# Optimization experiments

Measured on AMD Instinct MI355X. Metric: run time of the kernel, lower is better.

The kernel has to match this reference:

```python
import jax, jax.numpy as jnp
import numpy as np
from math import sqrt

B, L, S, H, E, D = 2, 2048, 2048, 16, 64, 64

def setup_inputs() -> dict:
    key = jax.random.key(0)
    kq, kk, kv = jax.random.split(key, 3)
    queries = jax.random.normal(kq, (B, L, H, E), dtype=jnp.float32)
    keys = jax.random.normal(kk, (B, S, H, E), dtype=jnp.float32)
    values = jax.random.normal(kv, (B, S, H, D), dtype=jnp.float32)
    # causal mask: True where attention is NOT allowed (j > i), matching masked_fill_ semantics
    causal = jnp.triu(jnp.ones((L, S), dtype=jnp.bool_), k=1)
    attn_mask = jnp.broadcast_to(causal[None, None, :, :], (B, 1, L, S))
    return {"queries": queries, "keys": keys, "values": values, "attn_mask": attn_mask}

def reference(queries, keys, values, attn_mask):
    # scores: [B,H,L,S]
    scale = 1.0 / sqrt(queries.shape[-1])
    scores = jnp.einsum('blhe,bshe->bhls', queries, keys)
    scores = jnp.where(attn_mask, -jnp.inf, scores)
    A = jax.nn.softmax(scale * scores, axis=-1)
    V = jnp.einsum('bhls,bshd->blhd', A, values)
    return V
```

## Files before the change

### kernel.cpp

```cpp
#include <hip/hip_runtime.h>

typedef unsigned short ushort_t;
typedef __attribute__((ext_vector_type(8))) short s8v;
typedef __attribute__((ext_vector_type(2))) unsigned u2v;
typedef __attribute__((ext_vector_type(4))) float f4;

__device__ __forceinline__ ushort_t f2bf(float x) {
    unsigned u = __builtin_bit_cast(unsigned, x);
    return (ushort_t)((u + 0x7FFFu + ((u >> 16) & 1u)) >> 16);
}
__device__ __forceinline__ unsigned pack_hi16(float lo, float hi) {
    unsigned a = __builtin_bit_cast(unsigned, lo);
    unsigned b = __builtin_bit_cast(unsigned, hi);
    return (a >> 16) | (b & 0xFFFF0000u);
}

__global__ __launch_bounds__(256) void prep_kv(const float* __restrict__ K,
                                               const float* __restrict__ V,
                                               ushort_t* __restrict__ Kb,
                                               ushort_t* __restrict__ VT) {
    __shared__ ushort_t T[64 * 72];
    if (blockIdx.x < 2048) {
        const int gid = blockIdx.x * 256 + threadIdx.x;
        const int e = (gid & 7) * 8;
        const int h = (gid >> 3) & 15;
        const int s = (gid >> 7) & 2047;
        const int b = gid >> 18;
        const float* src = K + (((b * 2048 + s) * 16 + h) * 64 + e);
        f4 a = *(const f4*)src;
        f4 c = *(const f4*)(src + 4);
        s8v o;
        #pragma unroll
        for (int j = 0; j < 4; ++j) { o[j] = (short)f2bf(a[j]); o[j + 4] = (short)f2bf(c[j]); }
        *(s8v*)(Kb + (((b * 16 + h) * 2048 + s) * 64 + e)) = o;
    } else {
        const int v = blockIdx.x - 2048;
        const int s0 = (v & 31) * 64;
        const int h  = (v >> 5) & 15;
        const int b  = v >> 9;
        const int t  = threadIdx.x;
        {
            const int srow = t >> 2, dc = (t & 3) * 16;
            const float* src = V + (((b * 2048 + s0 + srow) * 16 + h) * 64 + dc);
            #pragma unroll
            for (int c = 0; c < 4; ++c) {
                f4 vv = *(const f4*)(src + c * 4);
                #pragma unroll
                for (int j = 0; j < 4; ++j) T[(dc + c * 4 + j) * 72 + srow] = f2bf(vv[j]);
            }
        }
        __syncthreads();
        {
            const int d = t >> 2, sq = (t & 3) * 16;
            ushort_t* dst = VT + (((b * 16 + h) * 64 + d) * 2048 + s0 + sq);
            *(s8v*)(dst)     = *(const s8v*)(&T[d * 72 + sq]);
            *(s8v*)(dst + 8) = *(const s8v*)(&T[d * 72 + sq + 8]);
        }
    }
}

__global__ __launch_bounds__(256, 4) void fattn_main(
    const float* __restrict__ Q,
    const ushort_t* __restrict__ Kb,
    const ushort_t* __restrict__ VTb,
    float* __restrict__ O)
{
    constexpr float K1 = 0.18033688011112042f;
    constexpr float SHIFT = 12.0f;
    __shared__ ushort_t P[8][16 * 72];
    __shared__ float Obuf[32 * 64];
    __shared__ float Lbuf[32];

    const int bx = blockIdx.x;
    const int bh = bx & 31;
    const int pr = bx >> 5;
    const int b = bh >> 4, h = bh & 15;

    const int wave = threadIdx.x >> 6;
    const int lane = threadIdx.x & 63;
    const int l15  = lane & 15;
    const int quad = lane >> 4;

    const ushort_t* kb  = Kb  + bh * (2048 * 64);
    const ushort_t* vtb = VTb + bh * (64 * 2048);
    const float*    qb  = Q + b * (2048 * 1024) + h * 64;
    float*          ob  = O + b * (2048 * 1024) + h * 64;

    const s8v ones = {0x3F80, 0x3F80, 0x3F80, 0x3F80, 0x3F80, 0x3F80, 0x3F80, 0x3F80};
    const f4 zero4 = {0.f, 0.f, 0.f, 0.f};

    for (int half = 0; half < 2; ++half) {
        const int i   = half ? (63 - pr) : pr;
        const int qr0 = i * 32;
        const int il  = i >> 1;

        s8v aq[2][2];
        #pragma unroll
        for (int m = 0; m < 2; ++m) {
            const float* qrow = qb + (qr0 + m * 16 + l15) * 1024;
            #pragma unroll
            for (int ks = 0; ks < 2; ++ks) {
                f4 x = *(const f4*)(qrow + ks * 32 + quad * 8);
                f4 y = *(const f4*)(qrow + ks * 32 + quad * 8 + 4);
                #pragma unroll
                for (int j = 0; j < 4; ++j) {
                    aq[m][ks][j]     = (short)f2bf(x[j]);
                    aq[m][ks][j + 4] = (short)f2bf(y[j]);
                }
            }
        }

        f4 oacc[2][4];
        f4 lsum[2] = {zero4, zero4};
        #pragma unroll
        for (int m = 0; m < 2; ++m)
            #pragma unroll
            for (int d = 0; d < 4; ++d) oacc[m][d] = zero4;

        for (int it = wave; it <= il; it += 4) {
            const int n0 = it * 64;
            const ushort_t* kp = kb + n0 * 64;
            const ushort_t* vp = vtb + n0;

            s8v bk[4][2];
            #pragma unroll
            for (int t = 0; t < 4; ++t)
                #pragma unroll
                for (int ks = 0; ks < 2; ++ks)
                    bk[t][ks] = *(const s8v*)(kp + (t * 16 + l15) * 64 + ks * 32 + quad * 8);
            s8v bv[4][2];
            #pragma unroll
            for (int dd = 0; dd < 4; ++dd)
                #pragma unroll
                for (int ks = 0; ks < 2; ++ks)
                    bv[dd][ks] = *(const s8v*)(vp + (dd * 16 + l15) * 2048 + ks * 32 + quad * 8);

            const bool diag = (it == il);

            #pragma unroll
            for (int m = 0; m < 2; ++m) {
                ushort_t* Pm = P[wave * 2 + m];
                #pragma unroll
                for (int t = 0; t < 4; ++t) {
                    f4 a  = __builtin_amdgcn_mfma_f32_16x16x32_bf16(bk[t][0], aq[m][0], zero4, 0, 0, 0);
                    f4 st = __builtin_amdgcn_mfma_f32_16x16x32_bf16(bk[t][1], aq[m][1], a, 0, 0, 0);
                    float p[4];
                    #pragma unroll
                    for (int r = 0; r < 4; ++r) {
                        float x = __builtin_fmaf(st[r], K1, -SHIFT);
                        if (diag) {
                            const int gj = n0 + t * 16 + quad * 4 + r;
                            const int gi = qr0 + m * 16 + l15;
                            if (gj > gi) x = -INFINITY;
                        }
                        p[r] = __builtin_exp2f(x);
                    }
                    u2v pk;
                    pk[0] = pack_hi16(p[0], p[1]);
                    pk[1] = pack_hi16(p[2], p[3]);
                    *(u2v*)&Pm[l15 * 72 + t * 16 + quad * 4] = pk;
                }
            }

            #pragma unroll
            for (int m = 0; m < 2; ++m) {
                const ushort_t* Pm = P[wave * 2 + m];
                #pragma unroll
                for (int ks = 0; ks < 2; ++ks) {
                    const s8v ap = *(const s8v*)&Pm[l15 * 72 + ks * 32 + quad * 8];
                    lsum[m] = __builtin_amdgcn_mfma_f32_16x16x32_bf16(ap, ones, lsum[m], 0, 0, 0);
                    #pragma unroll
                    for (int dd = 0; dd < 4; ++dd)
                        oacc[m][dd] = __builtin_amdgcn_mfma_f32_16x16x32_bf16(ap, bv[dd][ks], oacc[m][dd], 0, 0, 0);
                }
            }
        }

        __syncthreads();
        #pragma unroll
        for (int w = 0; w < 4; ++w) {
            if (wave == w) {
                #pragma unroll
                for (int m = 0; m < 2; ++m) {
                    #pragma unroll
                    for (int dd = 0; dd < 4; ++dd)
                        #pragma unroll
                        for (int r = 0; r < 4; ++r) {
                            const int idx = (m * 16 + quad * 4 + r) * 64 + dd * 16 + l15;
                            if (w == 0) Obuf[idx] = oacc[m][dd][r];
                            else        Obuf[idx] += oacc[m][dd][r];
                        }
                    if (l15 == 0)
                        #pragma unroll
                        for (int r = 0; r < 4; ++r) {
                            const int row = m * 16 + quad * 4 + r;
                            if (w == 0) Lbuf[row] = lsum[m][r];
                            else        Lbuf[row] += lsum[m][r];
                        }
                }
            }
            __syncthreads();
        }
        {
            const int row = wave * 8 + (lane >> 3);
            const int c0  = (lane & 7) * 8;
            const float inv = 1.0f / Lbuf[row];
            f4 o0 = *(const f4*)&Obuf[row * 64 + c0];
            f4 o1 = *(const f4*)&Obuf[row * 64 + c0 + 4];
            #pragma unroll
            for (int j = 0; j < 4; ++j) { o0[j] *= inv; o1[j] *= inv; }
            float* dst = ob + (qr0 + row) * 1024 + c0;
            *(f4*)dst       = o0;
            *(f4*)(dst + 4) = o1;
        }
    }
}

#define PSTR 72
__global__ __launch_bounds__(256) void fattn_fallback(
    const float* __restrict__ Q, const float* __restrict__ K,
    const float* __restrict__ V, float* __restrict__ O)
{
    constexpr int strL = 1024, strB = 2048 * strL;
    const float scale = 0.125f;
    __shared__ ushort_t KT[64 * PSTR];
    __shared__ ushort_t VT[64 * PSTR];
    __shared__ ushort_t P[4][16 * PSTR];
    const int bh = blockIdx.x & 31;
    const int b = bh >> 4, h = bh & 15;
    const int im = 31 - (blockIdx.x >> 5);
    const int q0 = im * 64;
    const int tid = threadIdx.x, wave = tid >> 6, lane = tid & 63;
    const int l15 = lane & 15, quad = lane >> 4;
    const float* qbase = Q + b*strB + (q0 + wave*16 + l15)*strL + h*64;
    s8v aq0, aq1;
    {
        f4 q0v = *(const f4*)(qbase + quad*8);
        f4 q1v = *(const f4*)(qbase + quad*8 + 4);
        f4 q2v = *(const f4*)(qbase + 32 + quad*8);
        f4 q3v = *(const f4*)(qbase + 32 + quad*8 + 4);
        #pragma unroll
        for (int j = 0; j < 4; ++j) {
            aq0[j] = (short)f2bf(q0v[j]); aq0[j+4] = (short)f2bf(q1v[j]);
            aq1[j] = (short)f2bf(q2v[j]); aq1[j+4] = (short)f2bf(q3v[j]);
        }
    }
    const f4 zero4 = {0.f,0.f,0.f,0.f};
    f4 oacc[4]; float m_prev[4], lsum[4];
    #pragma unroll
    for (int d = 0; d < 4; ++d) oacc[d] = zero4;
    #pragma unroll
    for (int r = 0; r < 4; ++r) { m_prev[r] = -INFINITY; lsum[r] = 0.0f; }
    const float* kh = K + b*strB + h*64;
    const float* vh = V + b*strB + h*64;
    for (int it = 0; it <= im; ++it) {
        const int n0 = it * 64;
        __syncthreads();
        {
            const float* krow = kh + (n0 + lane)*strL + wave*16;
            f4 k0 = *(const f4*)(krow); f4 k1 = *(const f4*)(krow+4);
            f4 k2 = *(const f4*)(krow+8); f4 k3 = *(const f4*)(krow+12);
            s8v kb0, kb1;
            #pragma unroll
            for (int j = 0; j < 4; ++j) {
                kb0[j] = (short)f2bf(k0[j]); kb0[j+4] = (short)f2bf(k1[j]);
                kb1[j] = (short)f2bf(k2[j]); kb1[j+4] = (short)f2bf(k3[j]);
            }
            *(s8v*)&KT[lane*PSTR + wave*16] = kb0;
            *(s8v*)&KT[lane*PSTR + wave*16 + 8] = kb1;
            const float* vrow = vh + (n0 + lane)*strL + wave*16;
            f4 v0 = *(const f4*)(vrow); f4 v1 = *(const f4*)(vrow+4);
            f4 v2 = *(const f4*)(vrow+8); f4 v3 = *(const f4*)(vrow+12);
            #pragma unroll
            for (int j = 0; j < 4; ++j) {
                VT[(wave*16 + j)*PSTR + lane] = f2bf(v0[j]);
                VT[(wave*16 + 4 + j)*PSTR + lane] = f2bf(v1[j]);
                VT[(wave*16 + 8 + j)*PSTR + lane] = f2bf(v2[j]);
                VT[(wave*16 + 12 + j)*PSTR + lane] = f2bf(v3[j]);
            }
        }
        __syncthreads();
        f4 sacc[4];
        #pragma unroll
        for (int t = 0; t < 4; ++t) {
            sacc[t] = zero4;
            const s8v bk0 = *(const s8v*)&KT[(t*16 + l15)*PSTR + quad*8];
            const s8v bk1 = *(const s8v*)&KT[(t*16 + l15)*PSTR + 32 + quad*8];
            sacc[t] = __builtin_amdgcn_mfma_f32_16x16x32_bf16(aq0, bk0, sacc[t], 0, 0, 0);
            sacc[t] = __builtin_amdgcn_mfma_f32_16x16x32_bf16(aq1, bk1, sacc[t], 0, 0, 0);
        }
        const bool diag = (it == im);
        float sv[4][4], rmax[4];
        #pragma unroll
        for (int r = 0; r < 4; ++r) rmax[r] = -INFINITY;
        #pragma unroll
        for (int t = 0; t < 4; ++t)
            #pragma unroll
            for (int r = 0; r < 4; ++r) {
                float x = sacc[t][r] * scale;
                if (diag) {
                    const int gi = wave*16 + quad*4 + r;
                    const int gj = t*16 + l15;
                    if (gj > gi) x = -INFINITY;
                }
                sv[t][r] = x; rmax[r] = fmaxf(rmax[r], x);
            }
        #pragma unroll
        for (int off = 8; off >= 1; off >>= 1)
            #pragma unroll
            for (int r = 0; r < 4; ++r)
                rmax[r] = fmaxf(rmax[r], __shfl_xor(rmax[r], off, 64));
        float mnew[4], alpha[4], rsum[4];
        #pragma unroll
        for (int r = 0; r < 4; ++r) {
            mnew[r] = fmaxf(m_prev[r], rmax[r]);
            alpha[r] = __expf(m_prev[r] - mnew[r]);
            m_prev[r] = mnew[r]; rsum[r] = 0.f;
        }
        #pragma unroll
        for (int t = 0; t < 4; ++t)
            #pragma unroll
            for (int r = 0; r < 4; ++r) {
                const float p = __expf(sv[t][r] - mnew[r]);
                rsum[r] += p;
                P[wave][(quad*4 + r)*PSTR + t*16 + l15] = f2bf(p);
            }
        #pragma unroll
        for (int off = 8; off >= 1; off >>= 1)
            #pragma unroll
            for (int r = 0; r < 4; ++r)
                rsum[r] += __shfl_xor(rsum[r], off, 64);
        #pragma unroll
        for (int r = 0; r < 4; ++r) lsum[r] = alpha[r]*lsum[r] + rsum[r];
        #pragma unroll
        for (int d = 0; d < 4; ++d)
            #pragma unroll
            for (int r = 0; r < 4; ++r) oacc[d][r] *= alpha[r];
        #pragma unroll
        for (int ks = 0; ks < 2; ++ks) {
            const s8v ap = *(const s8v*)&P[wave][l15*PSTR + ks*32 + quad*8];
            #pragma unroll
            for (int d = 0; d < 4; ++d) {
                const s8v bvv = *(const s8v*)&VT[(d*16 + l15)*PSTR + ks*32 + quad*8];
                oacc[d] = __builtin_amdgcn_mfma_f32_16x16x32_bf16(ap, bvv, oacc[d], 0, 0, 0);
            }
        }
    }
    float* obase = O + b*strB + h*64;
    #pragma unroll
    for (int r = 0; r < 4; ++r) {
        const float inv = 1.0f / lsum[r];
        const int gi = q0 + wave*16 + quad*4 + r;
        #pragma unroll
        for (int d = 0; d < 4; ++d)
            obase[gi*strL + d*16 + l15] = oacc[d][r] * inv;
    }
}

extern "C" void kernel_launch(void* const* d_in, const int* in_sizes, int n_in,
                              void* d_out, int out_size, void* d_ws, size_t ws_size,
                              hipStream_t stream) {
    const float* Q = (const float*)d_in[0];
    const float* K = (const float*)d_in[1];
    const float* V = (const float*)d_in[2];
    float* O = (float*)d_out;
    const size_t NEED = 2ull * 4194304ull * 2ull;
    if (ws_size >= NEED) {
        ushort_t* Kb = (ushort_t*)d_ws;
        ushort_t* VT = Kb + 4194304;
        prep_kv<<<3072, 256, 0, stream>>>(K, V, Kb, VT);
        fattn_main<<<1024, 256, 0, stream>>>(Q, Kb, VT, O);
    } else {
        fattn_fallback<<<1024, 256, 0, stream>>>(Q, K, V, O);
    }
}
```

Before: 183.7 us.

## Share double-buffered K/V tiles in LDS across waves instead of splitting KV

The attention kernel changes from four waves each taking a strided subset of KV blocks (with a cross-wave reduction through shared memory) to two waves each owning 32 query rows of a 64-row tile. All waves now stream every KV block through double-buffered LDS tiles loaded cooperatively, with the next block prefetched while the current one is computed. The goal is to remove the Obuf/Lbuf reduction and its barriers, and to reuse each K/V load across more query rows. In exchange the grid has half as many blocks with 128 threads each, which lowers parallelism and occupancy. A barrier is also added on every KV iteration.

```diff
diff --git a/kernel.cpp b/kernel.cpp
--- a/kernel.cpp
+++ b/kernel.cpp
@@ -59,7 +59,7 @@
     }
 }
 
-__global__ __launch_bounds__(256, 4) void fattn_main(
+__global__ __launch_bounds__(128, 2) void fattn_main(
     const float* __restrict__ Q,
     const ushort_t* __restrict__ Kb,
     const ushort_t* __restrict__ VTb,
@@ -67,9 +67,9 @@
 {
     constexpr float K1 = 0.18033688011112042f;
     constexpr float SHIFT = 12.0f;
-    __shared__ ushort_t P[8][16 * 72];
-    __shared__ float Obuf[32 * 64];
-    __shared__ float Lbuf[32];
+    __shared__ ushort_t KT [2][64 * 72];
+    __shared__ ushort_t VTl[2][64 * 72];
+    __shared__ ushort_t P  [4][16 * 72];
 
     const int bx = blockIdx.x;
     const int bh = bx & 31;
@@ -89,15 +89,18 @@
     const s8v ones = {0x3F80, 0x3F80, 0x3F80, 0x3F80, 0x3F80, 0x3F80, 0x3F80, 0x3F80};
     const f4 zero4 = {0.f, 0.f, 0.f, 0.f};
 
+    const int sr = (wave << 5) + (lane >> 1);
+    const int sc = (lane & 1) << 5;
+
     for (int half = 0; half < 2; ++half) {
-        const int i   = half ? (63 - pr) : pr;
-        const int qr0 = i * 32;
-        const int il  = i >> 1;
+        const int i   = half ? (31 - pr) : pr;
+        const int qr0 = i * 64;
+        const int il  = i;
 
         s8v aq[2][2];
         #pragma unroll
         for (int m = 0; m < 2; ++m) {
-            const float* qrow = qb + (qr0 + m * 16 + l15) * 1024;
+            const float* qrow = qb + (qr0 + wave * 32 + m * 16 + l15) * 1024;
             #pragma unroll
             for (int ks = 0; ks < 2; ++ks) {
                 f4 x = *(const f4*)(qrow + ks * 32 + quad * 8);
@@ -117,40 +120,61 @@
             #pragma unroll
             for (int d = 0; d < 4; ++d) oacc[m][d] = zero4;
 
-        for (int it = wave; it <= il; it += 4) {
-            const int n0 = it * 64;
-            const ushort_t* kp = kb + n0 * 64;
-            const ushort_t* vp = vtb + n0;
-
-            s8v bk[4][2];
-            #pragma unroll
-            for (int t = 0; t < 4; ++t)
-                #pragma unroll
-                for (int ks = 0; ks < 2; ++ks)
-                    bk[t][ks] = *(const s8v*)(kp + (t * 16 + l15) * 64 + ks * 32 + quad * 8);
-            s8v bv[4][2];
-            #pragma unroll
-            for (int dd = 0; dd < 4; ++dd)
-                #pragma unroll
-                for (int ks = 0; ks < 2; ++ks)
-                    bv[dd][ks] = *(const s8v*)(vp + (dd * 16 + l15) * 2048 + ks * 32 + quad * 8);
-
+        {
+            const ushort_t* ksrc = kb + sr * 64 + sc;
+            ushort_t* kdst = &KT[0][sr * 72 + sc];
+            const ushort_t* vsrc = vtb + sr * 2048 + sc;
+            ushort_t* vdst = &VTl[0][sr * 72 + sc];
+            #pragma unroll
+            for (int c = 0; c < 4; ++c) {
+                *(s8v*)(kdst + c * 8) = *(const s8v*)(ksrc + c * 8);
+                *(s8v*)(vdst + c * 8) = *(const s8v*)(vsrc + c * 8);
+            }
+        }
+        __syncthreads();
+
+        for (int it = 0; it <= il; ++it) {
+            const int cur = it & 1;
+            const int n0  = it * 64;
             const bool diag = (it == il);
+
+            if (it < il) {
+                const int nn = (it + 1) * 64;
+                const ushort_t* ksrc = kb + (nn + sr) * 64 + sc;
+                ushort_t* kdst = &KT[cur ^ 1][sr * 72 + sc];
+                const ushort_t* vsrc = vtb + sr * 2048 + nn + sc;
+                ushort_t* vdst = &VTl[cur ^ 1][sr * 72 + sc];
+                #pragma unroll
+                for (int c = 0; c < 4; ++c) {
+                    *(s8v*)(kdst + c * 8) = *(const s8v*)(ksrc + c * 8);
+                    *(s8v*)(vdst + c * 8) = *(const s8v*)(vsrc + c * 8);
+                }
+            }
+
+            f4 st[2][4];
+            #pragma unroll
+            for (int t = 0; t < 4; ++t) {
+                const s8v bk0 = *(const s8v*)&KT[cur][(t * 16 + l15) * 72 + quad * 8];
+                const s8v bk1 = *(const s8v*)&KT[cur][(t * 16 + l15) * 72 + 32 + quad * 8];
+                #pragma unroll
+                for (int m = 0; m < 2; ++m) {
+                    f4 a = __builtin_amdgcn_mfma_f32_16x16x32_bf16(bk0, aq[m][0], zero4, 0, 0, 0);
+                    st[m][t] = __builtin_amdgcn_mfma_f32_16x16x32_bf16(bk1, aq[m][1], a, 0, 0, 0);
+                }
+            }
 
             #pragma unroll
             for (int m = 0; m < 2; ++m) {
                 ushort_t* Pm = P[wave * 2 + m];
                 #pragma unroll
                 for (int t = 0; t < 4; ++t) {
-                    f4 a  = __builtin_amdgcn_mfma_f32_16x16x32_bf16(bk[t][0], aq[m][0], zero4, 0, 0, 0);
-                    f4 st = __builtin_amdgcn_mfma_f32_16x16x32_bf16(bk[t][1], aq[m][1], a, 0, 0, 0);
                     float p[4];
                     #pragma unroll
                     for (int r = 0; r < 4; ++r) {
-                        float x = __builtin_fmaf(st[r], K1, -SHIFT);
+                        float x = __builtin_fmaf(st[m][t][r], K1, -SHIFT);
                         if (diag) {
                             const int gj = n0 + t * 16 + quad * 4 + r;
-                            const int gi = qr0 + m * 16 + l15;
+                            const int gi = qr0 + wave * 32 + m * 16 + l15;
                             if (gj > gi) x = -INFINITY;
                         }
                         p[r] = __builtin_exp2f(x);
@@ -170,49 +194,26 @@
                     const s8v ap = *(const s8v*)&Pm[l15 * 72 + ks * 32 + quad * 8];
                     lsum[m] = __builtin_amdgcn_mfma_f32_16x16x32_bf16(ap, ones, lsum[m], 0, 0, 0);
                     #pragma unroll
-                    for (int dd = 0; dd < 4; ++dd)
-                        oacc[m][dd] = __builtin_amdgcn_mfma_f32_16x16x32_bf16(ap, bv[dd][ks], oacc[m][dd], 0, 0, 0);
-                }
-            }
-        }
-
-        __syncthreads();
-        #pragma unroll
-        for (int w = 0; w < 4; ++w) {
-            if (wave == w) {
-                #pragma unroll
-                for (int m = 0; m < 2; ++m) {
-                    #pragma unroll
-                    for (int dd = 0; dd < 4; ++dd)
-                        #pragma unroll
-                        for (int r = 0; r < 4; ++r) {
-                            const int idx = (m * 16 + quad * 4 + r) * 64 + dd * 16 + l15;
-                            if (w == 0) Obuf[idx] = oacc[m][dd][r];
-                            else        Obuf[idx] += oacc[m][dd][r];
-                        }
-                    if (l15 == 0)
-                        #pragma unroll
-                        for (int r = 0; r < 4; ++r) {
-                            const int row = m * 16 + quad * 4 + r;
-                            if (w == 0) Lbuf[row] = lsum[m][r];
-                            else        Lbuf[row] += lsum[m][r];
-                        }
-                }
-            }
+                    for (int dd = 0; dd < 4; ++dd) {
+                        const s8v bv = *(const s8v*)&VTl[cur][(dd * 16 + l15) * 72 + ks * 32 + quad * 8];
+                        oacc[m][dd] = __builtin_amdgcn_mfma_f32_16x16x32_bf16(ap, bv, oacc[m][dd], 0, 0, 0);
+                    }
+                }
+            }
+
             __syncthreads();
         }
-        {
-            const int row = wave * 8 + (lane >> 3);
-            const int c0  = (lane & 7) * 8;
-            const float inv = 1.0f / Lbuf[row];
-            f4 o0 = *(const f4*)&Obuf[row * 64 + c0];
-            f4 o1 = *(const f4*)&Obuf[row * 64 + c0 + 4];
-            #pragma unroll
-            for (int j = 0; j < 4; ++j) { o0[j] *= inv; o1[j] *= inv; }
-            float* dst = ob + (qr0 + row) * 1024 + c0;
-            *(f4*)dst       = o0;
-            *(f4*)(dst + 4) = o1;
-        }
+
+        #pragma unroll
+        for (int m = 0; m < 2; ++m)
+            #pragma unroll
+            for (int r = 0; r < 4; ++r) {
+                const float inv = 1.0f / lsum[m][r];
+                const int row = qr0 + wave * 32 + m * 16 + quad * 4 + r;
+                #pragma unroll
+                for (int dd = 0; dd < 4; ++dd)
+                    ob[row * 1024 + dd * 16 + l15] = oacc[m][dd][r] * inv;
+            }
     }
 }
 
@@ -369,7 +370,7 @@
         ushort_t* Kb = (ushort_t*)d_ws;
         ushort_t* VT = Kb + 4194304;
         prep_kv<<<3072, 256, 0, stream>>>(K, V, Kb, VT);
-        fattn_main<<<1024, 256, 0, stream>>>(Q, Kb, VT, O);
+        fattn_main<<<512, 128, 0, stream>>>(Q, Kb, VT, O);
     } else {
         fattn_fallback<<<1024, 256, 0, stream>>>(Q, K, V, O);
     }
```

Result: faster. 167.9 us (-8.6%).
